# Kernel tuning notes

Measured on AMD Instinct MI355X. Metric: run time of the kernel, lower is better.

## Reference

```python
import jax, jax.numpy as jnp
import numpy as np

B, S, I, H = 16, 2048, 1024, 1024

def setup_inputs() -> dict:
    key = jax.random.key(0)
    ks = jax.random.split(key, 6)
    scale_ih = 1.0 / np.sqrt(I)
    scale_hh = 1.0 / np.sqrt(H)
    return {
        "x": jax.random.normal(ks[0], (B, S, I), dtype=jnp.float32),
        "hx": jax.random.normal(ks[1], (B, H), dtype=jnp.float32),
        "W_ih": jax.random.normal(ks[2], (H, I), dtype=jnp.float32) * scale_ih,
        "W_hh": jax.random.normal(ks[3], (H, H), dtype=jnp.float32) * scale_hh,
        "b_ih": jax.random.normal(ks[4], (H,), dtype=jnp.float32) * scale_ih,
        "b_hh": jax.random.normal(ks[5], (H,), dtype=jnp.float32) * scale_hh,
    }

def reference(x, hx, W_ih, W_hh, b_ih, b_hh):
    # Faithful to RecurrentCellWrapper: the Python loop passes the SAME
    # initial hx to the cell at every timestep (hx is never updated),
    # so all steps are independent and fully vectorizable.
    # cell: h' = tanh(x_t @ W_ih^T + b_ih + hx @ W_hh^T + b_hh)
    h_term = hx @ W_hh.T + b_hh + b_ih            # [B, H], shared across steps
    x_term = jnp.einsum('bsi,hi->bsh', x, W_ih)   # [B, S, H]
    out = jnp.tanh(x_term + h_term[:, None, :])   # [B, S, H]
    # batch_first=True: output already [batch, seq, hidden]
    return out
```

## Files before the change

### kernel.cpp

```cpp
#include <hip/hip_runtime.h>
#include <hip/hip_bf16.h>
#include <stdint.h>


#define M_TOT 32768
#define N_TOT 1024
#define K_TOT 1024

typedef short short8 __attribute__((ext_vector_type(8)));
typedef float f32x4  __attribute__((ext_vector_type(4)));

#define WS_XBF_OFF   0
#define WS_WBF_OFF   67108864
#define WS_HT_OFF    69206016

__device__ __forceinline__ unsigned short f32_to_bf16_rne(float f) {
    union { float f; unsigned int u; } v; v.f = f;
    unsigned int u = v.u;
    unsigned int r = u + 0x7fffu + ((u >> 16) & 1u);
    return (unsigned short)(r >> 16);
}

__device__ __forceinline__ float fast_tanh(float z) {
    float e = __expf(2.0f * z);
    return 1.0f - 2.0f / (e + 1.0f);
}

__global__ void prep_kernel(const float* __restrict__ x,
                            const float* __restrict__ wih,
                            const float* __restrict__ hx,
                            const float* __restrict__ whh,
                            const float* __restrict__ bih,
                            const float* __restrict__ bhh,
                            unsigned short* __restrict__ xbf,
                            unsigned short* __restrict__ wbf,
                            float* __restrict__ ht) {
    if (blockIdx.x < 2048) {
        const int NXV = 33554432 / 8;
        const int NWV = 1048576 / 8;
        const int stride = 2048 * 256;
        for (int v = blockIdx.x * 256 + threadIdx.x; v < NXV + NWV; v += stride) {
            const float* src; unsigned short* dst; long long base;
            if (v < NXV) { src = x;   dst = xbf; base = (long long)v * 8; }
            else         { src = wih; dst = wbf; base = (long long)(v - NXV) * 8; }
            float4 a = *(const float4*)(src + base);
            float4 b = *(const float4*)(src + base + 4);
            union { unsigned short s[8]; uint4 u; } o;
            o.s[0] = f32_to_bf16_rne(a.x); o.s[1] = f32_to_bf16_rne(a.y);
            o.s[2] = f32_to_bf16_rne(a.z); o.s[3] = f32_to_bf16_rne(a.w);
            o.s[4] = f32_to_bf16_rne(b.x); o.s[5] = f32_to_bf16_rne(b.y);
            o.s[6] = f32_to_bf16_rne(b.z); o.s[7] = f32_to_bf16_rne(b.w);
            *(uint4*)(dst + base) = o.u;
        }
    } else {
        int lane = threadIdx.x & 63;
        int w    = threadIdx.x >> 6;
        int wg_base = (blockIdx.x - 2048) * 8 + w * 2;
#pragma unroll
        for (int d = 0; d < 2; ++d) {
            int wg = wg_base + d;
            int b = wg >> 10, h = wg & 1023;
            const float* hr = hx  + (long long)b * 1024;
            const float* wr = whh + (long long)h * 1024;
            float s = 0.f;
#pragma unroll
            for (int p = 0; p < 4; ++p) {
                int idx = p * 256 + lane * 4;
                float4 a = *(const float4*)(hr + idx);
                float4 c = *(const float4*)(wr + idx);
                s += a.x * c.x + a.y * c.y + a.z * c.z + a.w * c.w;
            }
#pragma unroll
            for (int dd = 32; dd > 0; dd >>= 1) s += __shfl_down(s, dd, 64);
            if (lane == 0) ht[wg] = s + bih[h] + bhh[h];
        }
    }
}

#define GLDS16(gp, lp) \
    __builtin_amdgcn_global_load_lds((const __attribute__((address_space(1))) void*)(gp), \
                                     (__attribute__((address_space(3))) void*)(lp), 16, 0, 0)

#define KITER(KNEXT, P, STAGE)                                                 \
  {                                                                            \
    if (STAGE) {                                                               \
      GLDS16(gA0 + (KNEXT), lA0 + ((P) ^ 1) * 16384);                          \
      GLDS16(gA1 + (KNEXT), lA1 + ((P) ^ 1) * 16384);                          \
      GLDS16(gB0 + (KNEXT), lB0 + ((P) ^ 1) * 16384);                          \
      GLDS16(gB1 + (KNEXT), lB1 + ((P) ^ 1) * 16384);                          \
    }                                                                          \
    {                                                                          \
      const char* lb = lds + (P) * 16384;                                      \
      short8 af[4], bfr[4];                                                    \
      _Pragma("unroll")                                                        \
      for (int t4 = 0; t4 < 4; ++t4) {                                         \
        af[t4]  = *(const short8*)(lb + offA[t4]);                             \
        bfr[t4] = *(const short8*)(lb + offB[t4]);                             \
      }                                                                        \
      _Pragma("unroll")                                                        \
      for (int mt = 0; mt < 4; ++mt)                                           \
        _Pragma("unroll")                                                      \
        for (int nt = 0; nt < 4; ++nt)                                         \
          acc[mt][nt] = __builtin_amdgcn_mfma_f32_16x16x32_bf16(               \
              af[mt], bfr[nt], acc[mt][nt], 0, 0, 0);                          \
    }                                                                          \
    __syncthreads();                                                           \
  }

__global__ __launch_bounds__(256) void gemm_tanh_kernel(
    const unsigned short* __restrict__ A,
    const unsigned short* __restrict__ Bm,
    const float* __restrict__ ht,
    float* __restrict__ out)
{
    __shared__ __align__(16) char lds[32768];

    const int tid = threadIdx.x;
    const int w = tid >> 6, l = tid & 63;

    const int bid  = blockIdx.x;
    const int widx = (bid & 7) * 256 + (bid >> 3);
    const int tile_m = widx >> 3;
    const int tile_n = widx & 7;
    const int m0 = tile_m << 7, n0 = tile_n << 7;

    const int r0 = (w * 2 + 0) * 16 + (l >> 2);
    const int r1 = (w * 2 + 1) * 16 + (l >> 2);
    const int slot = l & 3;
    const int qg0 = (slot - (r0 >> 1)) & 3;
    const int qg1 = (slot - (r1 >> 1)) & 3;
    const unsigned short* gA0 = A  + (long long)(m0 + r0) * K_TOT + qg0 * 8;
    const unsigned short* gA1 = A  + (long long)(m0 + r1) * K_TOT + qg1 * 8;
    const unsigned short* gB0 = Bm + (long long)(n0 + r0) * K_TOT + qg0 * 8;
    const unsigned short* gB1 = Bm + (long long)(n0 + r1) * K_TOT + qg1 * 8;
    char* lA0 = lds + (w * 2 + 0) * 1024;
    char* lA1 = lds + (w * 2 + 1) * 1024;
    char* lB0 = lds + 8192 + (w * 2 + 0) * 1024;
    char* lB1 = lds + 8192 + (w * 2 + 1) * 1024;

    const int wm = w & 1, wn = w >> 1;
    const int lm = l & 15, q = l >> 4;
    int offA[4], offB[4];
#pragma unroll
    for (int t = 0; t < 4; ++t) {
        int rr = wm * 64 + t * 16 + lm;
        offA[t] = rr * 64 + (((q + (rr >> 1)) & 3) << 4);
        int nn = wn * 64 + t * 16 + lm;
        offB[t] = 8192 + nn * 64 + (((q + (nn >> 1)) & 3) << 4);
    }

    f32x4 acc[4][4];
#pragma unroll
    for (int i = 0; i < 4; ++i)
#pragma unroll
        for (int j = 0; j < 4; ++j)
            acc[i][j] = (f32x4){0.f, 0.f, 0.f, 0.f};

    GLDS16(gA0, lA0);
    GLDS16(gA1, lA1);
    GLDS16(gB0, lB0);
    GLDS16(gB1, lB1);
    __syncthreads();

    for (int i = 0; i < 30; i += 2) {
        KITER((i + 1) * 32, 0, true);
        KITER((i + 2) * 32, 1, true);
    }
    KITER(31 * 32, 0, true);
    KITER(0,       1, false);

    const int b = tile_m >> 4;
    float htv[4];
#pragma unroll
    for (int nt = 0; nt < 4; ++nt)
        htv[nt] = ht[b * 1024 + n0 + wn * 64 + nt * 16 + lm];

#pragma unroll
    for (int mt = 0; mt < 4; ++mt) {
#pragma unroll
        for (int nt = 0; nt < 4; ++nt) {
            int n = n0 + wn * 64 + nt * 16 + lm;
#pragma unroll
            for (int r = 0; r < 4; ++r) {
                int m = m0 + wm * 64 + mt * 16 + q * 4 + r;
                float z = acc[mt][nt][r] + htv[nt];
                out[(long long)m * N_TOT + n] = fast_tanh(z);
            }
        }
    }
}

extern "C" void kernel_launch(void* const* d_in, const int* in_sizes, int n_in,
                              void* d_out, int out_size, void* d_ws, size_t ws_size,
                              hipStream_t stream) {
    const float* x    = (const float*)d_in[0];
    const float* hx   = (const float*)d_in[1];
    const float* wih  = (const float*)d_in[2];
    const float* whh  = (const float*)d_in[3];
    const float* bih  = (const float*)d_in[4];
    const float* bhh  = (const float*)d_in[5];
    float* out = (float*)d_out;

    unsigned short* xbf = (unsigned short*)((char*)d_ws + WS_XBF_OFF);
    unsigned short* wbf = (unsigned short*)((char*)d_ws + WS_WBF_OFF);
    float*          htp = (float*)((char*)d_ws + WS_HT_OFF);

    prep_kernel<<<4096, 256, 0, stream>>>(x, wih, hx, whh, bih, bhh, xbf, wbf, htp);
    gemm_tanh_kernel<<<2048, 256, 0, stream>>>(xbf, wbf, htp, out);
}
```

Baseline: 330.2 us.

## Triple-buffer GEMM K-loop with partial vmcnt waits instead of full sync

Extends the LDS staging from two to three buffers so global-to-LDS loads are issued two K-steps ahead. The __syncthreads is replaced with an s_waitcnt vmcnt(4) plus a raw barrier, so the most recent stage's loads stay in flight while computing. This hides more memory latency but raises LDS per block from 32KB to 48KB, which can reduce blocks resident per CU.

```diff
diff --git a/kernel.cpp b/kernel.cpp
--- a/kernel.cpp
+++ b/kernel.cpp
@@ -81,16 +81,17 @@
     __builtin_amdgcn_global_load_lds((const __attribute__((address_space(1))) void*)(gp), \
                                      (__attribute__((address_space(3))) void*)(lp), 16, 0, 0)
 
-#define KITER(KNEXT, P, STAGE)                                                 \
+#define KITER(T, PC, PS, DOSTAGE, NW)                                          \
   {                                                                            \
-    if (STAGE) {                                                               \
-      GLDS16(gA0 + (KNEXT), lA0 + ((P) ^ 1) * 16384);                          \
-      GLDS16(gA1 + (KNEXT), lA1 + ((P) ^ 1) * 16384);                          \
-      GLDS16(gB0 + (KNEXT), lB0 + ((P) ^ 1) * 16384);                          \
-      GLDS16(gB1 + (KNEXT), lB1 + ((P) ^ 1) * 16384);                          \
+    if (DOSTAGE) {                                                             \
+      const int kk = ((T) + 2) * 32;                                           \
+      GLDS16(gA0 + kk, lA0 + (PS) * 16384);                                    \
+      GLDS16(gA1 + kk, lA1 + (PS) * 16384);                                    \
+      GLDS16(gB0 + kk, lB0 + (PS) * 16384);                                    \
+      GLDS16(gB1 + kk, lB1 + (PS) * 16384);                                    \
     }                                                                          \
     {                                                                          \
-      const char* lb = lds + (P) * 16384;                                      \
+      const char* lb = lds + (PC) * 16384;                                     \
       short8 af[4], bfr[4];                                                    \
       _Pragma("unroll")                                                        \
       for (int t4 = 0; t4 < 4; ++t4) {                                         \
@@ -104,7 +105,9 @@
           acc[mt][nt] = __builtin_amdgcn_mfma_f32_16x16x32_bf16(               \
               af[mt], bfr[nt], acc[mt][nt], 0, 0, 0);                          \
     }                                                                          \
-    __syncthreads();                                                           \
+    asm volatile("s_waitcnt vmcnt(" #NW ")" ::: "memory");                     \
+    __builtin_amdgcn_s_barrier();                                              \
+    asm volatile("" ::: "memory");                                             \
   }
 
 __global__ __launch_bounds__(256) void gemm_tanh_kernel(
@@ -113,7 +116,7 @@
     const float* __restrict__ ht,
     float* __restrict__ out)
 {
-    __shared__ __align__(16) char lds[32768];
+    __shared__ __align__(16) char lds[49152];
 
     const int tid = threadIdx.x;
     const int w = tid >> 6, l = tid & 63;
@@ -156,18 +159,35 @@
         for (int j = 0; j < 4; ++j)
             acc[i][j] = (f32x4){0.f, 0.f, 0.f, 0.f};
 
-    GLDS16(gA0, lA0);
-    GLDS16(gA1, lA1);
-    GLDS16(gB0, lB0);
-    GLDS16(gB1, lB1);
-    __syncthreads();
-
-    for (int i = 0; i < 30; i += 2) {
-        KITER((i + 1) * 32, 0, true);
-        KITER((i + 2) * 32, 1, true);
-    }
-    KITER(31 * 32, 0, true);
-    KITER(0,       1, false);
+    GLDS16(gA0 +  0, lA0);          GLDS16(gA1 +  0, lA1);
+    GLDS16(gB0 +  0, lB0);          GLDS16(gB1 +  0, lB1);
+    GLDS16(gA0 + 32, lA0 + 16384);  GLDS16(gA1 + 32, lA1 + 16384);
+    GLDS16(gB0 + 32, lB0 + 16384);  GLDS16(gB1 + 32, lB1 + 16384);
+    asm volatile("s_waitcnt vmcnt(4)" ::: "memory");
+    __builtin_amdgcn_s_barrier();
+    asm volatile("" ::: "memory");
+
+    for (int i = 0; i < 30; i += 3) {
+        KITER(i + 0, 0, 2, true, 4);
+        KITER(i + 1, 1, 0, true, 4);
+        KITER(i + 2, 2, 1, true, 4);
+    }
+    KITER(30, 0, 0, false, 0);
+    {
+        const char* lb = lds + 1 * 16384;
+        short8 af[4], bfr[4];
+#pragma unroll
+        for (int t4 = 0; t4 < 4; ++t4) {
+            af[t4]  = *(const short8*)(lb + offA[t4]);
+            bfr[t4] = *(const short8*)(lb + offB[t4]);
+        }
+#pragma unroll
+        for (int mt = 0; mt < 4; ++mt)
+#pragma unroll
+            for (int nt = 0; nt < 4; ++nt)
+                acc[mt][nt] = __builtin_amdgcn_mfma_f32_16x16x32_bf16(
+                    af[mt], bfr[nt], acc[mt][nt], 0, 0, 0);
+    }
 
     const int b = tile_m >> 4;
     float htv[4];
```

Result: no change. 325.6 us (-1.4%).
